# Performance work log

Hardware: AMD Instinct MI355X
Metric: run time of the kernel (lower is better)

## Reference

```python
import jax, jax.numpy as jnp
import numpy as np

DIM = 768
NUM_HEADS = 12
HEAD_DIM = DIM // NUM_HEADS
B, N = 16, 784


def setup_inputs() -> dict:
    key = jax.random.key(0)
    k1, k2, k3, k4, k5 = jax.random.split(key, 5)
    x = jax.random.normal(k1, (B, N, DIM), dtype=jnp.float32)
    # Dense params (flax Dense: kernel [in, out], bias [out])
    Wqkv = jax.random.normal(k2, (DIM, 3 * DIM), dtype=jnp.float32) * (DIM ** -0.5)
    bqkv = jnp.zeros((3 * DIM,), dtype=jnp.float32)
    Wo = jax.random.normal(k3, (DIM, DIM), dtype=jnp.float32) * (DIM ** -0.5)
    bo = jnp.zeros((DIM,), dtype=jnp.float32)
    return {"x": x, "Wqkv": Wqkv, "bqkv": bqkv, "Wo": Wo, "bo": bo}


def reference(x, Wqkv, bqkv, Wo, bo):
    b, n, dim = x.shape
    # fused QKV projection
    qkv = jnp.einsum('bnd,df->bnf', x, Wqkv) + bqkv          # [b, n, 3*dim]
    qkv = qkv.reshape(b, n, 3, NUM_HEADS, HEAD_DIM)           # '(k h d)' split
    q, k, v = qkv[:, :, 0], qkv[:, :, 1], qkv[:, :, 2]        # [b, n, h, d]
    scale = HEAD_DIM ** -0.5
    # chunked/flash path computes exact softmax attention; same math, expressed densely
    scores = jnp.einsum('bihd,bjhd->bhij', q, k) * scale      # [b, h, n, n]
    attn = jax.nn.softmax(scores, axis=-1)
    out = jnp.einsum('bhij,bjhd->bihd', attn, v)              # [b, n, h, d]
    out = out.reshape(b, n, dim)                              # 'b n (h d)'
    return jnp.einsum('bnd,df->bnf', out, Wo) + bo
```

## Files before the change

kernel.cpp:

```cpp
#include <hip/hip_runtime.h>

#define DIM 768
#define NHEADS 12
#define HDIM 64
#define BB 16
#define NN 784
#define M_TOTAL (BB * NN)

typedef __attribute__((ext_vector_type(8))) _Float16 f16x8;
typedef __attribute__((ext_vector_type(4))) float f32x4;
typedef __attribute__((ext_vector_type(16))) float f32x16;

typedef __attribute__((address_space(3))) unsigned int lds_uint;
typedef __attribute__((address_space(1))) const unsigned int g_uint;
__device__ inline void gload_lds16(const void* g, void* l) {
    __builtin_amdgcn_global_load_lds((g_uint*)(uintptr_t)g,
                                     (lds_uint*)(uintptr_t)l, 16, 0, 0);
}

__global__ __launch_bounds__(256) void cvt_f16_kernel(
    const float* __restrict__ in, _Float16* __restrict__ out, int n)
{
    int i = (blockIdx.x * 256 + threadIdx.x) * 8;
    if (i >= n) return;
    float4 a = *(const float4*)&in[i];
    float4 b = *(const float4*)&in[i + 4];
    union { _Float16 h[8]; uint4 v; } o;
    o.h[0] = (_Float16)a.x; o.h[1] = (_Float16)a.y;
    o.h[2] = (_Float16)a.z; o.h[3] = (_Float16)a.w;
    o.h[4] = (_Float16)b.x; o.h[5] = (_Float16)b.y;
    o.h[6] = (_Float16)b.z; o.h[7] = (_Float16)b.w;
    *(uint4*)&out[i] = o.v;
}

__global__ __launch_bounds__(256) void transpose_f16_kernel(
    const float* __restrict__ W, _Float16* __restrict__ T, int K, int N)
{
    __shared__ float t[32][33];
    const int n0 = blockIdx.x * 32, k0 = blockIdx.y * 32;
    const int r = threadIdx.x >> 3, c4 = (threadIdx.x & 7) * 4;
    float4 v = *(const float4*)&W[(size_t)(k0 + r) * N + n0 + c4];
    t[r][c4 + 0] = v.x; t[r][c4 + 1] = v.y;
    t[r][c4 + 2] = v.z; t[r][c4 + 3] = v.w;
    __syncthreads();
    union { _Float16 h[4]; ushort4 v4; } o;
#pragma unroll
    for (int i = 0; i < 4; ++i) o.h[i] = (_Float16)t[c4 + i][r];
    *(ushort4*)&T[(size_t)(n0 + r) * K + k0 + c4] = o.v4;
}

template <int OUT_F16>
__global__ __launch_bounds__(256) void gemm_f16_kernel(
    const _Float16* __restrict__ A, const _Float16* __restrict__ B,
    const float* __restrict__ bias, void* __restrict__ Cout,
    int M, int N, int K)
{
    __shared__ _Float16 sA[128 * 64];
    __shared__ _Float16 sB[128 * 64];

    const int tid  = threadIdx.x;
    const int wave = tid >> 6;
    const int lane = tid & 63;

    const int nwg = gridDim.x * gridDim.y;
    const int lid = blockIdx.x + gridDim.x * blockIdx.y;
    const int cq  = nwg >> 3, cr = nwg & 7;
    const int xcd = lid & 7, ix = lid >> 3;
    const int wgid = (xcd < cr ? xcd * (cq + 1) : cr * (cq + 1) + (xcd - cr) * cq) + ix;
    const int gn = (wgid % gridDim.x) * 128;
    const int gm = (wgid / gridDim.x) * 128;

    const int wm = (wave & 1) * 64;
    const int wn = (wave >> 1) * 64;
    const int l31 = lane & 31;
    const int hi  = lane >> 5;

    const int srow = lane >> 3;
    const int scol = (((lane & 7) ^ (srow & 7)) * 8);

    f32x16 acc[2][2] = {};

    for (int k0 = 0; k0 < K; k0 += 64) {
        __syncthreads();
#pragma unroll
        for (int i = 0; i < 4; ++i) {
            const int rbase = wave * 32 + i * 8;
            gload_lds16(A + (size_t)(gm + rbase + srow) * K + k0 + scol,
                        &sA[rbase * 64]);
            gload_lds16(B + (size_t)(gn + rbase + srow) * K + k0 + scol,
                        &sB[rbase * 64]);
        }
        __syncthreads();

#pragma unroll
        for (int kk = 0; kk < 4; ++kk) {
            const int c = kk * 2 + hi;
            const int sw = (c ^ (l31 & 7)) * 8;
            f16x8 a[2], bf[2];
#pragma unroll
            for (int mt = 0; mt < 2; ++mt)
                a[mt] = *(const f16x8*)&sA[(wm + mt * 32 + l31) * 64 + sw];
#pragma unroll
            for (int nt = 0; nt < 2; ++nt)
                bf[nt] = *(const f16x8*)&sB[(wn + nt * 32 + l31) * 64 + sw];
#pragma unroll
            for (int mt = 0; mt < 2; ++mt)
#pragma unroll
                for (int nt = 0; nt < 2; ++nt)
                    acc[mt][nt] = __builtin_amdgcn_mfma_f32_32x32x16_f16(
                        a[mt], bf[nt], acc[mt][nt], 0, 0, 0);
        }
    }

#pragma unroll
    for (int nt = 0; nt < 2; ++nt) {
        const int col = gn + wn + nt * 32 + l31;
        const float bv = bias[col];
#pragma unroll
        for (int mt = 0; mt < 2; ++mt) {
            f32x16 v = acc[mt][nt];
#pragma unroll
            for (int reg = 0; reg < 16; ++reg) {
                const int row = gm + wm + mt * 32 + (reg & 3) + 8 * (reg >> 2) + 4 * hi;
                const float o = v[reg] + bv;
                if (OUT_F16)
                    ((_Float16*)Cout)[(size_t)row * N + col] = (_Float16)o;
                else
                    ((float*)Cout)[(size_t)row * N + col] = o;
            }
        }
    }
}

#define LOG2E_8 0.18033688f

#define LOAD_TILE(J0, TAIL)                                                    \
  {                                                                            \
    const int j0_ = (J0);                                                      \
    int jrowK = j0_ + sj;                                                      \
    if (TAIL && jrowK > NN - 1) jrowK = NN - 1;                                \
    const size_t kbase = (size_t)(b * NN + jrowK) * (3 * DIM) + DIM + h * HDIM;\
    k0v = *(const uint4*)&qkv[kbase + sg * 8];                                 \
    k1v = *(const uint4*)&qkv[kbase + sg * 8 + 32];                            \
    int vr0 = j0_ + 2 * jj, vr1 = j0_ + 2 * jj + 1;                            \
    if (TAIL) { if (vr0 > NN - 1) vr0 = NN - 1; if (vr1 > NN - 1) vr1 = NN - 1; } \
    va.v = *(const uint4*)&qkv[(size_t)(b * NN + vr0) * (3 * DIM) + 2 * DIM + h * HDIM + dsub]; \
    vc.v = *(const uint4*)&qkv[(size_t)(b * NN + vr1) * (3 * DIM) + 2 * DIM + h * HDIM + dsub]; \
  }

#define WRITE_TILE()                                                           \
  {                                                                            \
    *(uint4*)&Ks[sj][sg * 8]      = k0v;                                       \
    *(uint4*)&Ks[sj][sg * 8 + 32] = k1v;                                       \
    _Pragma("unroll")                                                          \
    for (int i = 0; i < 8; ++i) {                                              \
        union { _Float16 h2[2]; unsigned int u; } t;                           \
        t.h2[0] = va.h[i]; t.h2[1] = vc.h[i];                                  \
        *(unsigned int*)&Vt[dsub + i][pcol] = t.u;                             \
    }                                                                          \
  }

#define EXP_PACK(SV, G, J0_, TAIL)                                             \
  {                                                                            \
    float p0 = exp2f(SV[0]), p1 = exp2f(SV[1]);                                \
    float p2 = exp2f(SV[2]), p3 = exp2f(SV[3]);                                \
    if (TAIL && (J0_ + nt * 16) >= NN) { p0 = p1 = p2 = p3 = 0.f; }            \
    lpart[G] += (p0 + p1) + (p2 + p3);                                         \
    union { _Float16 h2[2]; unsigned int u; } c0, c1;                          \
    c0.h2[0] = (_Float16)p0; c0.h2[1] = (_Float16)p1;                          \
    c1.h2[0] = (_Float16)p2; c1.h2[1] = (_Float16)p3;                          \
    pk[G][nt][0] = c0.u; pk[G][nt][1] = c1.u;                                  \
  }

#define COMPUTE_TILE(J0, TAIL)                                                 \
  {                                                                            \
    unsigned int pk[2][4][2];                                                  \
    _Pragma("unroll")                                                          \
    for (int nt = 0; nt < 4; ++nt) {                                           \
        f16x8 kf0 = *(const f16x8*)&Ks[nt * 16 + l16][quad * 8];               \
        f16x8 kf1 = *(const f16x8*)&Ks[nt * 16 + l16][32 + quad * 8];          \
        f32x4 s0 = {}, s1 = {};                                                \
        s0 = __builtin_amdgcn_mfma_f32_16x16x32_f16(kf0, qfrag[0][0], s0, 0, 0, 0); \
        s0 = __builtin_amdgcn_mfma_f32_16x16x32_f16(kf1, qfrag[0][1], s0, 0, 0, 0); \
        s1 = __builtin_amdgcn_mfma_f32_16x16x32_f16(kf0, qfrag[1][0], s1, 0, 0, 0); \
        s1 = __builtin_amdgcn_mfma_f32_16x16x32_f16(kf1, qfrag[1][1], s1, 0, 0, 0); \
        EXP_PACK(s0, 0, J0, TAIL)                                              \
        EXP_PACK(s1, 1, J0, TAIL)                                              \
    }                                                                          \
    __builtin_amdgcn_s_setprio(1);                                             \
    _Pragma("unroll")                                                          \
    for (int pc = 0; pc < 2; ++pc) {                                           \
        union { unsigned int u[4]; f16x8 v; } pa0, pa1;                        \
        pa0.u[0] = pk[0][2 * pc][0];     pa0.u[1] = pk[0][2 * pc][1];          \
        pa0.u[2] = pk[0][2 * pc + 1][0]; pa0.u[3] = pk[0][2 * pc + 1][1];      \
        pa1.u[0] = pk[1][2 * pc][0];     pa1.u[1] = pk[1][2 * pc][1];          \
        pa1.u[2] = pk[1][2 * pc + 1][0]; pa1.u[3] = pk[1][2 * pc + 1][1];      \
        _Pragma("unroll")                                                      \
        for (int dt = 0; dt < 4; ++dt) {                                       \
            f16x8 vf = *(const f16x8*)&Vt[dt * 16 + l16][pc * 32 + quad * 8];  \
            O[0][dt] = __builtin_amdgcn_mfma_f32_16x16x32_f16(pa0.v, vf, O[0][dt], 0, 0, 0); \
            O[1][dt] = __builtin_amdgcn_mfma_f32_16x16x32_f16(pa1.v, vf, O[1][dt], 0, 0, 0); \
        }                                                                      \
    }                                                                          \
    __builtin_amdgcn_s_setprio(0);                                             \
  }

__global__ __launch_bounds__(256, 2) void attn_f16_kernel(
    const _Float16* __restrict__ qkv, _Float16* __restrict__ oat)
{
    const int L   = blockIdx.x + 7 * (blockIdx.y + NHEADS * blockIdx.z);
    const int xcd = L & 7, ixc = L >> 3;
    const int grp = xcd * 24 + ixc / 7;
    const int q0  = (ixc % 7) * 128;
    const int b   = grp / NHEADS;
    const int h   = grp % NHEADS;

    const int tid = threadIdx.x;
    const int wave = tid >> 6;
    const int lane = tid & 63;
    const int quad = lane >> 4;
    const int l16  = lane & 15;

    __shared__ _Float16 Ks[64][72];
    __shared__ _Float16 Vt[64][72];

    f16x8 qfrag[2][2];
#pragma unroll
    for (int g = 0; g < 2; ++g) {
        int qrow = q0 + wave * 32 + g * 16 + l16; if (qrow > NN - 1) qrow = NN - 1;
        size_t base = (size_t)(b * NN + qrow) * (3 * DIM) + h * HDIM;
        qfrag[g][0] = (*(const f16x8*)&qkv[base + quad * 8]) * (_Float16)LOG2E_8;
        qfrag[g][1] = (*(const f16x8*)&qkv[base + 32 + quad * 8]) * (_Float16)LOG2E_8;
    }

    const int sj = lane;
    const int sg = wave;
    const int jj   = lane & 31;
    const int dsub = sg * 16 + (lane >> 5) * 8;
    const int pcol = ((jj >> 4) << 5) | (((jj >> 1) & 3) << 3)
                   | (((jj >> 3) & 1) << 2) | ((jj & 1) << 1);

    f32x4 O[2][4] = {};
    float lpart[2] = {0.f, 0.f};

    uint4 k0v, k1v;
    union { uint4 v; _Float16 h[8]; } va, vc;

    LOAD_TILE(0, 0)
#pragma unroll 1
    for (int jt = 0; jt < 11; ++jt) {
        __syncthreads();
        WRITE_TILE()
        __syncthreads();
        LOAD_TILE((jt + 1) * 64, 0)
        COMPUTE_TILE(0, 0)
    }
    __syncthreads();
    WRITE_TILE()
    __syncthreads();
    LOAD_TILE(768, 1)
    COMPUTE_TILE(704, 0)
    __syncthreads();
    WRITE_TILE()
    __syncthreads();
    COMPUTE_TILE(768, 1)

#pragma unroll
    for (int g = 0; g < 2; ++g) {
        float t = lpart[g];
        t += __shfl_xor(t, 16);
        t += __shfl_xor(t, 32);
        float inv[4];
#pragma unroll
        for (int r = 0; r < 4; ++r)
            inv[r] = 1.0f / __shfl(t, quad * 4 + r, 16);
#pragma unroll
        for (int r = 0; r < 4; ++r) {
            const int q = q0 + wave * 32 + g * 16 + quad * 4 + r;
            if (q < NN) {
#pragma unroll
                for (int dt = 0; dt < 4; ++dt) {
                    const size_t base = (size_t)(b * NN + q) * DIM + h * HDIM + dt * 16 + l16;
                    oat[base] = (_Float16)(O[g][dt][r] * inv[r]);
                }
            }
        }
    }
}

extern "C" void kernel_launch(void* const* d_in, const int* in_sizes, int n_in,
                              void* d_out, int out_size, void* d_ws, size_t ws_size,
                              hipStream_t stream) {
    const float* x    = (const float*)d_in[0];
    const float* Wqkv = (const float*)d_in[1];
    const float* bqkv = (const float*)d_in[2];
    const float* Wo   = (const float*)d_in[3];
    const float* bo   = (const float*)d_in[4];
    float* out = (float*)d_out;

    _Float16* qkv = (_Float16*)d_ws;
    _Float16* xh  = qkv + (size_t)M_TOTAL * 3 * DIM;
    _Float16* wqT = xh + (size_t)M_TOTAL * DIM;
    _Float16* woT = wqT + (size_t)3 * DIM * DIM;
    _Float16* oat = xh;

    {
        int n = M_TOTAL * DIM;
        cvt_f16_kernel<<<n / 8 / 256, 256, 0, stream>>>(x, xh, n);
    }
    transpose_f16_kernel<<<dim3((3 * DIM) / 32, DIM / 32), 256, 0, stream>>>(
        Wqkv, wqT, DIM, 3 * DIM);
    transpose_f16_kernel<<<dim3(DIM / 32, DIM / 32), 256, 0, stream>>>(
        Wo, woT, DIM, DIM);
    gemm_f16_kernel<1><<<dim3((3 * DIM) / 128, M_TOTAL / 128), 256, 0, stream>>>(
        xh, wqT, bqkv, qkv, M_TOTAL, 3 * DIM, DIM);
    attn_f16_kernel<<<dim3(7, NHEADS, BB), 256, 0, stream>>>(qkv, oat);
    gemm_f16_kernel<0><<<dim3(DIM / 128, M_TOTAL / 128), 256, 0, stream>>>(
        oat, woT, bo, out, M_TOTAL, DIM, DIM);
}
```

Baseline: 255.7 us.

## Double-buffer K/V LDS tiles and use packed fp16 convert with dot2 row sums

```diff
diff --git a/kernel.cpp b/kernel.cpp
--- a/kernel.cpp
+++ b/kernel.cpp
@@ -10,12 +10,38 @@
 typedef __attribute__((ext_vector_type(8))) _Float16 f16x8;
 typedef __attribute__((ext_vector_type(4))) float f32x4;
 typedef __attribute__((ext_vector_type(16))) float f32x16;
+typedef __fp16 fp16x2 __attribute__((ext_vector_type(2)));
 
 typedef __attribute__((address_space(3))) unsigned int lds_uint;
 typedef __attribute__((address_space(1))) const unsigned int g_uint;
 __device__ inline void gload_lds16(const void* g, void* l) {
     __builtin_amdgcn_global_load_lds((g_uint*)(uintptr_t)g,
                                      (lds_uint*)(uintptr_t)l, 16, 0, 0);
+}
+
+#if __has_builtin(__builtin_amdgcn_exp2f)
+#define EXP2(x) __builtin_amdgcn_exp2f(x)
+#else
+#define EXP2(x) exp2f(x)
+#endif
+
+__device__ inline unsigned int pk2(float a, float b, float* lacc) {
+#if __has_builtin(__builtin_amdgcn_cvt_pkrtz)
+    union { fp16x2 h; unsigned int u; } r;
+    r.h = __builtin_amdgcn_cvt_pkrtz(a, b);
+#if __has_builtin(__builtin_amdgcn_fdot2)
+    const fp16x2 one = {(__fp16)1.f, (__fp16)1.f};
+    *lacc = __builtin_amdgcn_fdot2(r.h, one, *lacc, false);
+#else
+    *lacc += a + b;
+#endif
+    return r.u;
+#else
+    union { _Float16 h[2]; unsigned int u; } r;
+    r.h[0] = (_Float16)a; r.h[1] = (_Float16)b;
+    *lacc += a + b;
+    return r.u;
+#endif
 }
 
 __global__ __launch_bounds__(256) void cvt_f16_kernel(
@@ -148,37 +174,38 @@
     vc.v = *(const uint4*)&qkv[(size_t)(b * NN + vr1) * (3 * DIM) + 2 * DIM + h * HDIM + dsub]; \
   }
 
-#define WRITE_TILE()                                                           \
+#define WRITE_TILE(BUF)                                                        \
   {                                                                            \
-    *(uint4*)&Ks[sj][sg * 8]      = k0v;                                       \
-    *(uint4*)&Ks[sj][sg * 8 + 32] = k1v;                                       \
+    _Float16 (*K_)[72] = Ks[BUF];                                              \
+    _Float16 (*V_)[72] = Vt[BUF];                                              \
+    *(uint4*)&K_[sj][sg * 8]      = k0v;                                       \
+    *(uint4*)&K_[sj][sg * 8 + 32] = k1v;                                       \
     _Pragma("unroll")                                                          \
     for (int i = 0; i < 8; ++i) {                                              \
         union { _Float16 h2[2]; unsigned int u; } t;                           \
         t.h2[0] = va.h[i]; t.h2[1] = vc.h[i];                                  \
-        *(unsigned int*)&Vt[dsub + i][pcol] = t.u;                             \
+        *(unsigned int*)&V_[dsub + i][pcol] = t.u;                             \
     }                                                                          \
   }
 
 #define EXP_PACK(SV, G, J0_, TAIL)                                             \
   {                                                                            \
-    float p0 = exp2f(SV[0]), p1 = exp2f(SV[1]);                                \
-    float p2 = exp2f(SV[2]), p3 = exp2f(SV[3]);                                \
+    float p0 = EXP2(SV[0]), p1 = EXP2(SV[1]);                                  \
+    float p2 = EXP2(SV[2]), p3 = EXP2(SV[3]);                                  \
     if (TAIL && (J0_ + nt * 16) >= NN) { p0 = p1 = p2 = p3 = 0.f; }            \
-    lpart[G] += (p0 + p1) + (p2 + p3);                                         \
-    union { _Float16 h2[2]; unsigned int u; } c0, c1;                          \
-    c0.h2[0] = (_Float16)p0; c0.h2[1] = (_Float16)p1;                          \
-    c1.h2[0] = (_Float16)p2; c1.h2[1] = (_Float16)p3;                          \
-    pk[G][nt][0] = c0.u; pk[G][nt][1] = c1.u;                                  \
+    pk[G][nt][0] = pk2(p0, p1, &lpart[G]);                                     \
+    pk[G][nt][1] = pk2(p2, p3, &lpart[G]);                                     \
   }
 
-#define COMPUTE_TILE(J0, TAIL)                                                 \
+#define COMPUTE_TILE(BUF, J0, TAIL)                                            \
   {                                                                            \
+    _Float16 (*K_)[72] = Ks[BUF];                                              \
+    _Float16 (*V_)[72] = Vt[BUF];                                              \
     unsigned int pk[2][4][2];                                                  \
     _Pragma("unroll")                                                          \
     for (int nt = 0; nt < 4; ++nt) {                                           \
-        f16x8 kf0 = *(const f16x8*)&Ks[nt * 16 + l16][quad * 8];               \
-        f16x8 kf1 = *(const f16x8*)&Ks[nt * 16 + l16][32 + quad * 8];          \
+        f16x8 kf0 = *(const f16x8*)&K_[nt * 16 + l16][quad * 8];               \
+        f16x8 kf1 = *(const f16x8*)&K_[nt * 16 + l16][32 + quad * 8];          \
         f32x4 s0 = {}, s1 = {};                                                \
         s0 = __builtin_amdgcn_mfma_f32_16x16x32_f16(kf0, qfrag[0][0], s0, 0, 0, 0); \
         s0 = __builtin_amdgcn_mfma_f32_16x16x32_f16(kf1, qfrag[0][1], s0, 0, 0, 0); \
@@ -197,7 +224,7 @@
         pa1.u[2] = pk[1][2 * pc + 1][0]; pa1.u[3] = pk[1][2 * pc + 1][1];      \
         _Pragma("unroll")                                                      \
         for (int dt = 0; dt < 4; ++dt) {                                       \
-            f16x8 vf = *(const f16x8*)&Vt[dt * 16 + l16][pc * 32 + quad * 8];  \
+            f16x8 vf = *(const f16x8*)&V_[dt * 16 + l16][pc * 32 + quad * 8];  \
             O[0][dt] = __builtin_amdgcn_mfma_f32_16x16x32_f16(pa0.v, vf, O[0][dt], 0, 0, 0); \
             O[1][dt] = __builtin_amdgcn_mfma_f32_16x16x32_f16(pa1.v, vf, O[1][dt], 0, 0, 0); \
         }                                                                      \
@@ -221,8 +248,8 @@
     const int quad = lane >> 4;
     const int l16  = lane & 15;
 
-    __shared__ _Float16 Ks[64][72];
-    __shared__ _Float16 Vt[64][72];
+    __shared__ _Float16 Ks[2][64][72];
+    __shared__ _Float16 Vt[2][64][72];
 
     f16x8 qfrag[2][2];
 #pragma unroll
@@ -249,21 +276,18 @@
     LOAD_TILE(0, 0)
 #pragma unroll 1
     for (int jt = 0; jt < 11; ++jt) {
-        __syncthreads();
-        WRITE_TILE()
+        WRITE_TILE(jt & 1)
         __syncthreads();
         LOAD_TILE((jt + 1) * 64, 0)
-        COMPUTE_TILE(0, 0)
-    }
-    __syncthreads();
-    WRITE_TILE()
+        COMPUTE_TILE(jt & 1, 0, 0)
+    }
+    WRITE_TILE(1)
     __syncthreads();
     LOAD_TILE(768, 1)
-    COMPUTE_TILE(704, 0)
+    COMPUTE_TILE(1, 704, 0)
+    WRITE_TILE(0)
     __syncthreads();
-    WRITE_TILE()
-    __syncthreads();
-    COMPUTE_TILE(768, 1)
+    COMPUTE_TILE(0, 768, 1)
 
 #pragma unroll
     for (int g = 0; g < 2; ++g) {
```

Measured after the change: 241.2 us. -5.7%, faster.
